# Optimization experiments

Hardware: AMD Instinct MI355X
Metric: run time of the kernel (lower is better)

The kernel has to match this reference:

```python
import jax, jax.numpy as jnp
import numpy as np

D_MODEL = 512
NHEAD = 8
HEAD_DIM = D_MODEL // NHEAD
D_FF = 2048
EPS = 1e-5


def _layernorm(x, w, b):
    mu = jnp.mean(x, axis=-1, keepdims=True)
    var = jnp.mean(jnp.square(x - mu), axis=-1, keepdims=True)
    return (x - mu) * jax.lax.rsqrt(var + EPS) * w + b


def setup_inputs() -> dict:
    key = jax.random.key(0)
    ks = jax.random.split(key, 10)
    B, L = 4, 2048
    x = jax.random.normal(ks[0], (B, L, D_MODEL), dtype=jnp.float32)
    attn_bias = jax.random.normal(ks[1], (1, NHEAD, L, L), dtype=jnp.float32)
    s = 0.02
    # weights stored as (in, out): y = x @ w + b
    wq = jax.random.normal(ks[2], (D_MODEL, D_MODEL), dtype=jnp.float32) * s
    wk = jax.random.normal(ks[3], (D_MODEL, D_MODEL), dtype=jnp.float32) * s
    wv = jax.random.normal(ks[4], (D_MODEL, D_MODEL), dtype=jnp.float32) * s
    wo = jax.random.normal(ks[5], (D_MODEL, D_MODEL), dtype=jnp.float32) * s
    w1 = jax.random.normal(ks[6], (D_MODEL, D_FF), dtype=jnp.float32) * s
    w2 = jax.random.normal(ks[7], (D_FF, D_MODEL), dtype=jnp.float32) * s
    z = lambda n: jnp.zeros((n,), dtype=jnp.float32)
    o = lambda n: jnp.ones((n,), dtype=jnp.float32)
    return {
        "x": x, "attn_bias": attn_bias,
        "ln1_w": o(D_MODEL), "ln1_b": z(D_MODEL),
        "ln2_w": o(D_MODEL), "ln2_b": z(D_MODEL),
        "wq": wq, "bq": z(D_MODEL), "wk": wk, "bk": z(D_MODEL),
        "wv": wv, "bv": z(D_MODEL), "wo": wo, "bo": z(D_MODEL),
        "w1": w1, "b1": z(D_FF), "w2": w2, "b2": z(D_MODEL),
    }


def reference(x, attn_bias, ln1_w, ln1_b, ln2_w, ln2_b,
              wq, bq, wk, bk, wv, bv, wo, bo, w1, b1, w2, b2):
    B, L, D = x.shape
    H, Dh = NHEAD, HEAD_DIM

    # --- self-attention block (pre-LN) ---
    h = _layernorm(x, ln1_w, ln1_b)
    q = (h @ wq + bq).reshape(B, L, H, Dh)
    k = (h @ wk + bk).reshape(B, L, H, Dh)
    v = (h @ wv + bv).reshape(B, L, H, Dh)
    scores = jnp.einsum('bqhd,bkhd->bhqk', q, k) * (Dh ** -0.5)
    scores = scores + attn_bias  # broadcast over batch if bias has leading 1
    attn = jax.nn.softmax(scores, axis=-1)
    o = jnp.einsum('bhqk,bkhd->bqhd', attn, v).reshape(B, L, D)
    x = x + (o @ wo + bo)

    # --- feed-forward block (pre-LN, exact GELU like torch nn.GELU) ---
    h2 = _layernorm(x, ln2_w, ln2_b)
    ff = jax.nn.gelu(h2 @ w1 + b1, approximate=False) @ w2 + b2
    return x + ff
```

## Files before the change

kernel.cpp:

```cpp
#include <hip/hip_runtime.h>
#include <hip/hip_bf16.h>

typedef __bf16 bf16x8 __attribute__((ext_vector_type(8)));
typedef float  f32x4  __attribute__((ext_vector_type(4)));
typedef unsigned short us8 __attribute__((ext_vector_type(8)));

__device__ inline unsigned short f2bf(float f) {
    unsigned u = __builtin_bit_cast(unsigned, f);
    u += 0x7fffu + ((u >> 16) & 1u);
    return (unsigned short)(u >> 16);
}

__device__ inline bf16x8 load_frag(const unsigned short* p) {
    return *reinterpret_cast<const bf16x8*>(p);
}

__device__ inline void gload_lds16(const unsigned short* g, unsigned short* l) {
    __builtin_amdgcn_global_load_lds(
        (const __attribute__((address_space(1))) void*)g,
        (__attribute__((address_space(3))) void*)l, 16, 0, 0);
}

__global__ void prep_kernel(const float* __restrict__ wq, const float* __restrict__ wk,
                            const float* __restrict__ wv, const float* __restrict__ wo,
                            const float* __restrict__ w1, const float* __restrict__ w2,
                            const float* __restrict__ bq, const float* __restrict__ bk,
                            const float* __restrict__ bv,
                            unsigned short* __restrict__ wqkvT, unsigned short* __restrict__ woT,
                            unsigned short* __restrict__ w1T, unsigned short* __restrict__ w2T,
                            float* __restrict__ biasqkv) {
    int bid = blockIdx.x;
    int tx = threadIdx.x, ty = threadIdx.y;
    if (bid >= 3072) {
        int i = (bid - 3072) * 256 + ty * 32 + tx;
        float v = (i < 512) ? bq[i] : ((i < 1024) ? bk[i - 512] : bv[i - 1024]);
        biasqkv[i] = v;
        return;
    }
    const float* src; unsigned short* dst; int K, N, tile;
    if (bid < 256)       { src = wq; dst = wqkvT;          K = 512;  N = 512;  tile = bid; }
    else if (bid < 512)  { src = wk; dst = wqkvT + 262144; K = 512;  N = 512;  tile = bid - 256; }
    else if (bid < 768)  { src = wv; dst = wqkvT + 524288; K = 512;  N = 512;  tile = bid - 512; }
    else if (bid < 1024) { src = wo; dst = woT;            K = 512;  N = 512;  tile = bid - 768; }
    else if (bid < 2048) { src = w1; dst = w1T;            K = 512;  N = 2048; tile = bid - 1024; }
    else                 { src = w2; dst = w2T;            K = 2048; N = 512;  tile = bid - 2048; }
    int ntx = N >> 5;
    int n0 = (tile % ntx) * 32, k0 = (tile / ntx) * 32;
    __shared__ float tilebuf[32][33];
#pragma unroll
    for (int i = 0; i < 4; ++i)
        tilebuf[ty + 8 * i][tx] = src[(size_t)(k0 + ty + 8 * i) * N + n0 + tx];
    __syncthreads();
#pragma unroll
    for (int i = 0; i < 4; ++i)
        dst[(size_t)(n0 + ty + 8 * i) * K + k0 + tx] = f2bf(tilebuf[tx][ty + 8 * i]);
}

__global__ __launch_bounds__(256) void ln_kernel(const float* __restrict__ x,
                                                 const float* __restrict__ w,
                                                 const float* __restrict__ b,
                                                 unsigned short* __restrict__ out) {
    int wave = threadIdx.x >> 6, lane = threadIdx.x & 63;
    size_t row = (size_t)blockIdx.x * 4 + wave;
    const float* xp = x + row * 512 + lane * 8;
    float4 v0 = *reinterpret_cast<const float4*>(xp);
    float4 v1 = *reinterpret_cast<const float4*>(xp + 4);
    float s = (v0.x + v0.y) + (v0.z + v0.w) + (v1.x + v1.y) + (v1.z + v1.w);
    float qq = v0.x * v0.x + v0.y * v0.y + v0.z * v0.z + v0.w * v0.w
             + v1.x * v1.x + v1.y * v1.y + v1.z * v1.z + v1.w * v1.w;
#pragma unroll
    for (int off = 1; off < 64; off <<= 1) {
        s += __shfl_xor(s, off, 64);
        qq += __shfl_xor(qq, off, 64);
    }
    float mu = s * (1.0f / 512.0f);
    float var = qq * (1.0f / 512.0f) - mu * mu;
    float rstd = rsqrtf(var + 1e-5f);
    int c = lane * 8;
    float4 w0 = *reinterpret_cast<const float4*>(w + c);
    float4 w1 = *reinterpret_cast<const float4*>(w + c + 4);
    float4 b0 = *reinterpret_cast<const float4*>(b + c);
    float4 b1 = *reinterpret_cast<const float4*>(b + c + 4);
    us8 r;
    r[0] = f2bf((v0.x - mu) * rstd * w0.x + b0.x);
    r[1] = f2bf((v0.y - mu) * rstd * w0.y + b0.y);
    r[2] = f2bf((v0.z - mu) * rstd * w0.z + b0.z);
    r[3] = f2bf((v0.w - mu) * rstd * w0.w + b0.w);
    r[4] = f2bf((v1.x - mu) * rstd * w1.x + b1.x);
    r[5] = f2bf((v1.y - mu) * rstd * w1.y + b1.y);
    r[6] = f2bf((v1.z - mu) * rstd * w1.z + b1.z);
    r[7] = f2bf((v1.w - mu) * rstd * w1.w + b1.w);
    *reinterpret_cast<us8*>(out + row * 512 + c) = r;
}

__device__ __forceinline__ void gemm_core(const unsigned short* __restrict__ A,
                                          const unsigned short* __restrict__ BT,
                                          int K, int ksteps,
                                          int m0, int n0, f32x4 (&acc)[4][4]) {
    __shared__ unsigned short As[8192];
    __shared__ unsigned short Bs[8192];
    const int tid = threadIdx.x;
    const int lane = tid & 63, wave = tid >> 6;
    const int quad = lane >> 4, l16 = lane & 15;
    const int wm = (wave >> 1) * 64, wn = (wave & 1) * 64;
    const int row0 = tid >> 3;
    const int jl = (tid & 7) ^ (row0 & 7);
    const unsigned short* ag = A + (size_t)(m0 + row0) * K + jl * 8;
    const unsigned short* bg = BT + (size_t)(n0 + row0) * K + jl * 8;
    unsigned short* al = As + tid * 8;
    unsigned short* bl = Bs + tid * 8;
    const int sw = l16 & 7;

    for (int ks = 0; ks < ksteps; ++ks) {
        __syncthreads();
#pragma unroll
        for (int s = 0; s < 4; ++s) {
            gload_lds16(ag + (size_t)32 * s * K, al + 2048 * s);
            gload_lds16(bg + (size_t)32 * s * K, bl + 2048 * s);
        }
        ag += 64; bg += 64;
        __syncthreads();
#pragma unroll
        for (int h = 0; h < 2; ++h) {
            bf16x8 af[4], bf[4];
#pragma unroll
            for (int i = 0; i < 4; ++i)
                af[i] = load_frag(As + (wm + i * 16 + l16) * 64 + (((h * 4 + quad) ^ sw) * 8));
#pragma unroll
            for (int j = 0; j < 4; ++j)
                bf[j] = load_frag(Bs + (wn + j * 16 + l16) * 64 + (((h * 4 + quad) ^ sw) * 8));
#pragma unroll
            for (int i = 0; i < 4; ++i)
#pragma unroll
                for (int j = 0; j < 4; ++j)
                    acc[i][j] = __builtin_amdgcn_mfma_f32_16x16x32_bf16(af[i], bf[j], acc[i][j], 0, 0, 0);
        }
    }
}

__device__ __forceinline__ void gemm_core_n64(const unsigned short* __restrict__ A,
                                              const unsigned short* __restrict__ BT,
                                              int K, int ksteps,
                                              int m0, int n0, f32x4 (&acc)[2][4]) {
    __shared__ unsigned short As[8192];
    __shared__ unsigned short Bs[4096];
    const int tid = threadIdx.x;
    const int lane = tid & 63, wave = tid >> 6;
    const int quad = lane >> 4, l16 = lane & 15;
    const int wm = wave * 32;
    const int row0 = tid >> 3;
    const int jl = (tid & 7) ^ (row0 & 7);
    const unsigned short* ag = A + (size_t)(m0 + row0) * K + jl * 8;
    const unsigned short* bg = BT + (size_t)(n0 + (row0 & 31)) * K + jl * 8;
    unsigned short* al = As + tid * 8;
    unsigned short* bl = Bs + tid * 8;
    const bool bstage = (row0 < 32);
    (void)bstage;
    const int sw = l16 & 7;

    for (int ks = 0; ks < ksteps; ++ks) {
        __syncthreads();
#pragma unroll
        for (int s = 0; s < 4; ++s)
            gload_lds16(ag + (size_t)32 * s * K, al + 2048 * s);
#pragma unroll
        for (int s = 0; s < 2; ++s)
            gload_lds16(bg + (size_t)32 * s * K, bl + 2048 * s);
        ag += 64; bg += 64;
        __syncthreads();
#pragma unroll
        for (int h = 0; h < 2; ++h) {
            bf16x8 af[2], bf[4];
#pragma unroll
            for (int i = 0; i < 2; ++i)
                af[i] = load_frag(As + (wm + i * 16 + l16) * 64 + (((h * 4 + quad) ^ sw) * 8));
#pragma unroll
            for (int j = 0; j < 4; ++j)
                bf[j] = load_frag(Bs + (j * 16 + l16) * 64 + (((h * 4 + quad) ^ sw) * 8));
#pragma unroll
            for (int i = 0; i < 2; ++i)
#pragma unroll
                for (int j = 0; j < 4; ++j)
                    acc[i][j] = __builtin_amdgcn_mfma_f32_16x16x32_bf16(af[i], bf[j], acc[i][j], 0, 0, 0);
        }
    }
}


__global__ __launch_bounds__(256) void gemm_oproj(const unsigned short* __restrict__ A,
                                                  const unsigned short* __restrict__ BT,
                                                  const float* __restrict__ bias,
                                                  const float* __restrict__ res,
                                                  float* __restrict__ C) {
    f32x4 acc[2][4] = {};
    const int m0 = blockIdx.y * 128, n0 = blockIdx.x * 64;
    gemm_core_n64(A, BT, 512, 8, m0, n0, acc);
    const int tid = threadIdx.x, lane = tid & 63, wave = tid >> 6;
    const int quad = lane >> 4, l16 = lane & 15;
    const int wm = wave * 32;
#pragma unroll
    for (int i = 0; i < 2; ++i)
#pragma unroll
        for (int j = 0; j < 4; ++j) {
            int n = n0 + j * 16 + l16;
            float bn = bias[n];
#pragma unroll
            for (int r = 0; r < 4; ++r) {
                int m = m0 + wm + i * 16 + quad * 4 + r;
                size_t idx = (size_t)m * 512 + n;
                C[idx] = acc[i][j][r] + bn + res[idx];
            }
        }
}

__global__ __launch_bounds__(256) void gemm_ff2(const unsigned short* __restrict__ A,
                                                const unsigned short* __restrict__ BT,
                                                const float* __restrict__ bias,
                                                float* __restrict__ C) {
    f32x4 acc[2][4] = {};
    const int m0 = blockIdx.y * 128, n0 = blockIdx.x * 64;
    gemm_core_n64(A, BT, 2048, 32, m0, n0, acc);
    const int tid = threadIdx.x, lane = tid & 63, wave = tid >> 6;
    const int quad = lane >> 4, l16 = lane & 15;
    const int wm = wave * 32;
#pragma unroll
    for (int i = 0; i < 2; ++i)
#pragma unroll
        for (int j = 0; j < 4; ++j) {
            int n = n0 + j * 16 + l16;
            float bn = bias[n];
#pragma unroll
            for (int r = 0; r < 4; ++r) {
                int m = m0 + wm + i * 16 + quad * 4 + r;
                size_t idx = (size_t)m * 512 + n;
                C[idx] = C[idx] + acc[i][j][r] + bn;
            }
        }
}

__global__ __launch_bounds__(256) void gemm_qkv_k(const unsigned short* __restrict__ A,
                                                  const unsigned short* __restrict__ BT,
                                                  const float* __restrict__ bias,
                                                  unsigned short* __restrict__ qk,
                                                  unsigned short* __restrict__ vT) {
    f32x4 acc[4][4] = {};
    const int m0 = blockIdx.y * 128, n0 = blockIdx.x * 128;
    gemm_core(A, BT, 512, 8, m0, n0, acc);
    const int tid = threadIdx.x, lane = tid & 63, wave = tid >> 6;
    const int quad = lane >> 4, l16 = lane & 15;
    const int wm = (wave >> 1) * 64, wn = (wave & 1) * 64;
    if (n0 < 1024) {
#pragma unroll
        for (int i = 0; i < 4; ++i)
#pragma unroll
            for (int j = 0; j < 4; ++j) {
                int n = n0 + wn + j * 16 + l16;
                float bn = bias[n];
#pragma unroll
                for (int r = 0; r < 4; ++r) {
                    int m = m0 + wm + i * 16 + quad * 4 + r;
                    qk[(size_t)m * 1024 + n] = f2bf(acc[i][j][r] + bn);
                }
            }
    } else {
#pragma unroll
        for (int i = 0; i < 4; ++i) {
            int mb = m0 + wm + i * 16 + quad * 4;
            int bb = mb >> 11, tok = mb & 2047;
#pragma unroll
            for (int j = 0; j < 4; ++j) {
                int n = n0 + wn + j * 16 + l16;
                float bn = bias[n];
                int hd = n - 1024;
                ushort4 pk;
                pk.x = f2bf(acc[i][j][0] + bn);
                pk.y = f2bf(acc[i][j][1] + bn);
                pk.z = f2bf(acc[i][j][2] + bn);
                pk.w = f2bf(acc[i][j][3] + bn);
                *reinterpret_cast<ushort4*>(vT + (size_t)(bb * 512 + hd) * 2048 + tok) = pk;
            }
        }
    }
}

__global__ __launch_bounds__(256) void gemm_gelu_k(const unsigned short* __restrict__ A,
                                                   const unsigned short* __restrict__ BT,
                                                   const float* __restrict__ bias,
                                                   unsigned short* __restrict__ C) {
    f32x4 acc[4][4] = {};
    const int m0 = blockIdx.y * 128, n0 = blockIdx.x * 128;
    gemm_core(A, BT, 512, 8, m0, n0, acc);
    const int tid = threadIdx.x, lane = tid & 63, wave = tid >> 6;
    const int quad = lane >> 4, l16 = lane & 15;
    const int wm = (wave >> 1) * 64, wn = (wave & 1) * 64;
#pragma unroll
    for (int i = 0; i < 4; ++i)
#pragma unroll
        for (int j = 0; j < 4; ++j) {
            int n = n0 + wn + j * 16 + l16;
            float bn = bias[n];
#pragma unroll
            for (int r = 0; r < 4; ++r) {
                int m = m0 + wm + i * 16 + quad * 4 + r;
                float val = acc[i][j][r] + bn;
                float g = 0.5f * val * (1.0f + erff(val * 0.70710678118654752f));
                C[(size_t)m * 2048 + n] = f2bf(g);
            }
        }
}

__global__ __launch_bounds__(256) void attn_kernel(const unsigned short* __restrict__ qk,
                                                   const unsigned short* __restrict__ vT,
                                                   const float* __restrict__ bias,
                                                   unsigned short* __restrict__ o) {
    __shared__ unsigned short Ks[2][2][4096];
    __shared__ unsigned short VTs[2][2][4096];
    __shared__ unsigned short Ps[2][4096];
    const int tid = threadIdx.x;
    const int lane = tid & 63, wave = tid >> 6, quad = lane >> 4, l16 = lane & 15;
    const int qb = blockIdx.x, h = blockIdx.y, bp = blockIdx.z;
    const int qw = qb * 64 + wave * 16;

    bf16x8 qf[2][2];
#pragma unroll
    for (int bi = 0; bi < 2; ++bi) {
        const unsigned short* qbase =
            qk + (size_t)((bp * 2 + bi) * 2048 + qw + l16) * 1024 + h * 64 + quad * 8;
        qf[bi][0] = load_frag(qbase);
        qf[bi][1] = load_frag(qbase + 32);
    }

    f32x4 Oacc[2][4] = {};
    float lsum[2][4] = {};

    const int p8 = lane & 7;
    const int r0 = wave * 16 + (lane >> 3);
    const int swz = (p8 ^ (r0 & 7)) * 8;
    const unsigned short* kg[2];
    const unsigned short* vg[2];
#pragma unroll
    for (int bi = 0; bi < 2; ++bi) {
        int b = bp * 2 + bi;
        kg[bi] = qk + (size_t)(b * 2048 + r0) * 1024 + 512 + h * 64 + swz;
        vg[bi] = vT + (size_t)(b * 512 + h * 64 + r0) * 2048 + swz;
    }
    const int ldst = r0 * 64 + p8 * 8;

    const float* brow = bias + (size_t)h * 2048 * 2048 + (size_t)(qw + quad * 4) * 2048 + l16;
    const float S2 = 0.18033688011112042f;
    const float K2 = 1.4426950408889634f;
    const float C2 = -11.541560327111707f;

#pragma unroll
    for (int bi = 0; bi < 2; ++bi) {
        gload_lds16(kg[bi], &Ks[0][bi][0] + ldst);
        gload_lds16(kg[bi] + 8 * 1024, &Ks[0][bi][512] + ldst);
        gload_lds16(vg[bi], &VTs[0][bi][0] + ldst);
        gload_lds16(vg[bi] + 8 * 2048, &VTs[0][bi][512] + ldst);
    }
    float bbf[4][4];
#pragma unroll
    for (int t = 0; t < 4; ++t)
#pragma unroll
        for (int r = 0; r < 4; ++r)
            bbf[t][r] = fmaf(brow[(size_t)r * 2048 + t * 16], K2, C2);

    const int sw7 = l16 & 7;
    for (int kt = 0; kt < 32; ++kt) {
        const int buf = kt & 1;
        __syncthreads();
        if (kt < 31) {
#pragma unroll
            for (int bi = 0; bi < 2; ++bi) {
                const unsigned short* kg2 = kg[bi] + (size_t)(kt + 1) * 64 * 1024;
                const unsigned short* vg2 = vg[bi] + (kt + 1) * 64;
                gload_lds16(kg2, &Ks[buf ^ 1][bi][0] + ldst);
                gload_lds16(kg2 + 8 * 1024, &Ks[buf ^ 1][bi][512] + ldst);
                gload_lds16(vg2, &VTs[buf ^ 1][bi][0] + ldst);
                gload_lds16(vg2 + 8 * 2048, &VTs[buf ^ 1][bi][512] + ldst);
            }
        }
#pragma unroll
        for (int bi = 0; bi < 2; ++bi) {
#pragma unroll
            for (int t = 0; t < 4; ++t) {
                const unsigned short* krow = &Ks[buf][bi][(t * 16 + l16) * 64];
                bf16x8 kb0 = load_frag(krow + ((quad ^ sw7) * 8));
                bf16x8 kb1 = load_frag(krow + (((quad + 4) ^ sw7) * 8));
                f32x4 c = {};
                c = __builtin_amdgcn_mfma_f32_16x16x32_bf16(qf[bi][0], kb0, c, 0, 0, 0);
                c = __builtin_amdgcn_mfma_f32_16x16x32_bf16(qf[bi][1], kb1, c, 0, 0, 0);
#pragma unroll
                for (int r = 0; r < 4; ++r) {
                    float e = __builtin_amdgcn_exp2f(fmaf(c[r], S2, bbf[t][r]));
                    lsum[bi][r] += e;
                    int m = quad * 4 + r;
                    int phys = (t * 2 + (l16 >> 3)) ^ ((m >> 1) & 7);
                    Ps[bi][wave * 1024 + m * 64 + phys * 8 + (l16 & 7)] = f2bf(e);
                }
            }
        }
        __syncthreads();
        if (kt < 31) {
            const float* b2 = brow + (size_t)(kt + 1) * 64;
#pragma unroll
            for (int t = 0; t < 4; ++t)
#pragma unroll
                for (int r = 0; r < 4; ++r)
                    bbf[t][r] = fmaf(b2[(size_t)r * 2048 + t * 16], K2, C2);
        }
#pragma unroll
        for (int bi = 0; bi < 2; ++bi) {
            const unsigned short* prow = &Ps[bi][wave * 1024 + l16 * 64];
            bf16x8 pa0 = load_frag(prow + ((quad ^ ((l16 >> 1) & 7)) * 8));
            bf16x8 pa1 = load_frag(prow + (((quad + 4) ^ ((l16 >> 1) & 7)) * 8));
#pragma unroll
            for (int t = 0; t < 4; ++t) {
                const unsigned short* vrow = &VTs[buf][bi][(t * 16 + l16) * 64];
                bf16x8 vb0 = load_frag(vrow + ((quad ^ sw7) * 8));
                bf16x8 vb1 = load_frag(vrow + (((quad + 4) ^ sw7) * 8));
                Oacc[bi][t] = __builtin_amdgcn_mfma_f32_16x16x32_bf16(pa0, vb0, Oacc[bi][t], 0, 0, 0);
                Oacc[bi][t] = __builtin_amdgcn_mfma_f32_16x16x32_bf16(pa1, vb1, Oacc[bi][t], 0, 0, 0);
            }
        }
    }

#pragma unroll
    for (int off = 1; off < 16; off <<= 1)
#pragma unroll
        for (int bi = 0; bi < 2; ++bi)
#pragma unroll
            for (int r = 0; r < 4; ++r) lsum[bi][r] += __shfl_xor(lsum[bi][r], off, 64);
#pragma unroll
    for (int bi = 0; bi < 2; ++bi)
#pragma unroll
        for (int r = 0; r < 4; ++r) {
            float inv = 1.0f / lsum[bi][r];
            int qg = qw + quad * 4 + r;
            unsigned short* op = o + (size_t)((bp * 2 + bi) * 2048 + qg) * 512 + h * 64;
#pragma unroll
            for (int t = 0; t < 4; ++t) op[t * 16 + l16] = f2bf(Oacc[bi][t][r] * inv);
        }
}

extern "C" void kernel_launch(void* const* d_in, const int* in_sizes, int n_in,
                              void* d_out, int out_size, void* d_ws, size_t ws_size,
                              hipStream_t stream) {
    const float* x      = (const float*)d_in[0];
    const float* abias  = (const float*)d_in[1];
    const float* ln1_w  = (const float*)d_in[2];
    const float* ln1_b  = (const float*)d_in[3];
    const float* ln2_w  = (const float*)d_in[4];
    const float* ln2_b  = (const float*)d_in[5];
    const float* wq     = (const float*)d_in[6];
    const float* bq     = (const float*)d_in[7];
    const float* wk     = (const float*)d_in[8];
    const float* bk     = (const float*)d_in[9];
    const float* wv     = (const float*)d_in[10];
    const float* bv     = (const float*)d_in[11];
    const float* wo     = (const float*)d_in[12];
    const float* bo     = (const float*)d_in[13];
    const float* w1     = (const float*)d_in[14];
    const float* b1     = (const float*)d_in[15];
    const float* w2     = (const float*)d_in[16];
    const float* b2     = (const float*)d_in[17];
    float* out = (float*)d_out;

    char* ws = (char*)d_ws;
    unsigned short* wqkvT  = (unsigned short*)(ws + 0);
    unsigned short* woT    = (unsigned short*)(ws + 1572864);
    unsigned short* w1T    = (unsigned short*)(ws + 2097152);
    unsigned short* w2T    = (unsigned short*)(ws + 4194304);
    float*          biasqkv= (float*)(ws + 6291456);
    unsigned short* hbuf   = (unsigned short*)(ws + 6297600);
    unsigned short* qkbuf  = (unsigned short*)(ws + 14686208);
    unsigned short* vTbuf  = (unsigned short*)(ws + 31463424);
    unsigned short* o_attn = (unsigned short*)(ws + 39852032);
    unsigned short* ff1    = (unsigned short*)(ws + 48240640);

    prep_kernel<<<3078, dim3(32, 8), 0, stream>>>(wq, wk, wv, wo, w1, w2, bq, bk, bv,
                                                  wqkvT, woT, w1T, w2T, biasqkv);
    ln_kernel<<<2048, 256, 0, stream>>>(x, ln1_w, ln1_b, hbuf);
    gemm_qkv_k<<<dim3(12, 64), 256, 0, stream>>>(hbuf, wqkvT, biasqkv, qkbuf, vTbuf);
    attn_kernel<<<dim3(32, 8, 2), 256, 0, stream>>>(qkbuf, vTbuf, abias, o_attn);
    gemm_oproj<<<dim3(8, 64), 256, 0, stream>>>(o_attn, woT, bo, x, out);
    ln_kernel<<<2048, 256, 0, stream>>>(out, ln2_w, ln2_b, hbuf);
    gemm_gelu_k<<<dim3(16, 64), 256, 0, stream>>>(hbuf, w1T, b1, ff1);
    gemm_ff2<<<dim3(8, 64), 256, 0, stream>>>(ff1, w2T, b2, out);
}
```

Before: 417.0 us.

## Double-buffer GEMM LDS tiles with prefetch and relax an attention barrier

Both GEMM cores switch from a single 64-wide K tile staged between two barriers per step to two 32-wide K buffers. The next tile is prefetched with direct global-to-LDS loads while MFMAs run on the current one, leaving one barrier per step. The LDS layout and XOR swizzle change to fit 32-element rows, and all callers double their step counts. In attention, one __syncthreads becomes a barrier that waits only on LDS counters, so outstanding global loads are not drained there. The price is twice as many loop iterations with half the MFMA work in each, and correctness now depends on the later full barrier catching the in-flight loads.

New measurement: 449.6 us. 1.08x slower.

```diff
diff --git a/kernel.cpp b/kernel.cpp
--- a/kernel.cpp
+++ b/kernel.cpp
@@ -19,6 +19,10 @@
     __builtin_amdgcn_global_load_lds(
         (const __attribute__((address_space(1))) void*)g,
         (__attribute__((address_space(3))) void*)l, 16, 0, 0);
+}
+
+__device__ inline void barrier_lds_only() {
+    asm volatile("s_waitcnt lgkmcnt(0)\ns_barrier" ::: "memory");
 }
 
 __global__ void prep_kernel(const float* __restrict__ wq, const float* __restrict__ wk,
@@ -97,44 +101,47 @@
                                           const unsigned short* __restrict__ BT,
                                           int K, int ksteps,
                                           int m0, int n0, f32x4 (&acc)[4][4]) {
-    __shared__ unsigned short As[8192];
-    __shared__ unsigned short Bs[8192];
+    __shared__ unsigned short As[2][4096];
+    __shared__ unsigned short Bs[2][4096];
     const int tid = threadIdx.x;
     const int lane = tid & 63, wave = tid >> 6;
     const int quad = lane >> 4, l16 = lane & 15;
     const int wm = (wave >> 1) * 64, wn = (wave & 1) * 64;
-    const int row0 = tid >> 3;
-    const int jl = (tid & 7) ^ (row0 & 7);
-    const unsigned short* ag = A + (size_t)(m0 + row0) * K + jl * 8;
-    const unsigned short* bg = BT + (size_t)(n0 + row0) * K + jl * 8;
-    unsigned short* al = As + tid * 8;
-    unsigned short* bl = Bs + tid * 8;
-    const int sw = l16 & 7;
+    const int c0 = tid, c1 = tid + 256;
+    const unsigned short* ag0 = A + (size_t)(m0 + (c0 >> 2)) * K + ((c0 & 3) ^ ((c0 >> 2) & 3)) * 8;
+    const unsigned short* ag1 = A + (size_t)(m0 + (c1 >> 2)) * K + ((c1 & 3) ^ ((c1 >> 2) & 3)) * 8;
+    const unsigned short* bg0 = BT + (size_t)(n0 + (c0 >> 2)) * K + ((c0 & 3) ^ ((c0 >> 2) & 3)) * 8;
+    const unsigned short* bg1 = BT + (size_t)(n0 + (c1 >> 2)) * K + ((c1 & 3) ^ ((c1 >> 2) & 3)) * 8;
+    const int l0 = c0 * 8, l1 = c1 * 8;
+    const int sw = (quad ^ (l16 & 3)) * 8;
+
+    gload_lds16(ag0, &As[0][0] + l0);
+    gload_lds16(ag1, &As[0][0] + l1);
+    gload_lds16(bg0, &Bs[0][0] + l0);
+    gload_lds16(bg1, &Bs[0][0] + l1);
 
     for (int ks = 0; ks < ksteps; ++ks) {
+        const int buf = ks & 1;
         __syncthreads();
-#pragma unroll
-        for (int s = 0; s < 4; ++s) {
-            gload_lds16(ag + (size_t)32 * s * K, al + 2048 * s);
-            gload_lds16(bg + (size_t)32 * s * K, bl + 2048 * s);
-        }
-        ag += 64; bg += 64;
-        __syncthreads();
-#pragma unroll
-        for (int h = 0; h < 2; ++h) {
-            bf16x8 af[4], bf[4];
-#pragma unroll
-            for (int i = 0; i < 4; ++i)
-                af[i] = load_frag(As + (wm + i * 16 + l16) * 64 + (((h * 4 + quad) ^ sw) * 8));
+        if (ks + 1 < ksteps) {
+            const int ko = (ks + 1) * 32;
+            gload_lds16(ag0 + ko, &As[buf ^ 1][0] + l0);
+            gload_lds16(ag1 + ko, &As[buf ^ 1][0] + l1);
+            gload_lds16(bg0 + ko, &Bs[buf ^ 1][0] + l0);
+            gload_lds16(bg1 + ko, &Bs[buf ^ 1][0] + l1);
+        }
+        bf16x8 af[4], bf[4];
+#pragma unroll
+        for (int i = 0; i < 4; ++i)
+            af[i] = load_frag(&As[buf][(wm + i * 16 + l16) * 32] + sw);
+#pragma unroll
+        for (int j = 0; j < 4; ++j)
+            bf[j] = load_frag(&Bs[buf][(wn + j * 16 + l16) * 32] + sw);
+#pragma unroll
+        for (int i = 0; i < 4; ++i)
 #pragma unroll
             for (int j = 0; j < 4; ++j)
-                bf[j] = load_frag(Bs + (wn + j * 16 + l16) * 64 + (((h * 4 + quad) ^ sw) * 8));
-#pragma unroll
-            for (int i = 0; i < 4; ++i)
-#pragma unroll
-                for (int j = 0; j < 4; ++j)
-                    acc[i][j] = __builtin_amdgcn_mfma_f32_16x16x32_bf16(af[i], bf[j], acc[i][j], 0, 0, 0);
-        }
+                acc[i][j] = __builtin_amdgcn_mfma_f32_16x16x32_bf16(af[i], bf[j], acc[i][j], 0, 0, 0);
     }
 }
 
@@ -142,50 +149,46 @@
                                               const unsigned short* __restrict__ BT,
                                               int K, int ksteps,
                                               int m0, int n0, f32x4 (&acc)[2][4]) {
-    __shared__ unsigned short As[8192];
-    __shared__ unsigned short Bs[4096];
+    __shared__ unsigned short As[2][4096];
+    __shared__ unsigned short Bs[2][2048];
     const int tid = threadIdx.x;
     const int lane = tid & 63, wave = tid >> 6;
     const int quad = lane >> 4, l16 = lane & 15;
     const int wm = wave * 32;
-    const int row0 = tid >> 3;
-    const int jl = (tid & 7) ^ (row0 & 7);
-    const unsigned short* ag = A + (size_t)(m0 + row0) * K + jl * 8;
-    const unsigned short* bg = BT + (size_t)(n0 + (row0 & 31)) * K + jl * 8;
-    unsigned short* al = As + tid * 8;
-    unsigned short* bl = Bs + tid * 8;
-    const bool bstage = (row0 < 32);
-    (void)bstage;
-    const int sw = l16 & 7;
+    const int c0 = tid, c1 = tid + 256;
+    const unsigned short* ag0 = A + (size_t)(m0 + (c0 >> 2)) * K + ((c0 & 3) ^ ((c0 >> 2) & 3)) * 8;
+    const unsigned short* ag1 = A + (size_t)(m0 + (c1 >> 2)) * K + ((c1 & 3) ^ ((c1 >> 2) & 3)) * 8;
+    const unsigned short* bg0 = BT + (size_t)(n0 + (c0 >> 2)) * K + ((c0 & 3) ^ ((c0 >> 2) & 3)) * 8;
+    const int l0 = c0 * 8, l1 = c1 * 8;
+    const int sw = (quad ^ (l16 & 3)) * 8;
+
+    gload_lds16(ag0, &As[0][0] + l0);
+    gload_lds16(ag1, &As[0][0] + l1);
+    gload_lds16(bg0, &Bs[0][0] + l0);
 
     for (int ks = 0; ks < ksteps; ++ks) {
+        const int buf = ks & 1;
         __syncthreads();
-#pragma unroll
-        for (int s = 0; s < 4; ++s)
-            gload_lds16(ag + (size_t)32 * s * K, al + 2048 * s);
-#pragma unroll
-        for (int s = 0; s < 2; ++s)
-            gload_lds16(bg + (size_t)32 * s * K, bl + 2048 * s);
-        ag += 64; bg += 64;
-        __syncthreads();
-#pragma unroll
-        for (int h = 0; h < 2; ++h) {
-            bf16x8 af[2], bf[4];
-#pragma unroll
-            for (int i = 0; i < 2; ++i)
-                af[i] = load_frag(As + (wm + i * 16 + l16) * 64 + (((h * 4 + quad) ^ sw) * 8));
+        if (ks + 1 < ksteps) {
+            const int ko = (ks + 1) * 32;
+            gload_lds16(ag0 + ko, &As[buf ^ 1][0] + l0);
+            gload_lds16(ag1 + ko, &As[buf ^ 1][0] + l1);
+            gload_lds16(bg0 + ko, &Bs[buf ^ 1][0] + l0);
+        }
+        bf16x8 af[2], bf[4];
+#pragma unroll
+        for (int i = 0; i < 2; ++i)
+            af[i] = load_frag(&As[buf][(wm + i * 16 + l16) * 32] + sw);
+#pragma unroll
+        for (int j = 0; j < 4; ++j)
+            bf[j] = load_frag(&Bs[buf][(j * 16 + l16) * 32] + sw);
+#pragma unroll
+        for (int i = 0; i < 2; ++i)
 #pragma unroll
             for (int j = 0; j < 4; ++j)
-                bf[j] = load_frag(Bs + (j * 16 + l16) * 64 + (((h * 4 + quad) ^ sw) * 8));
-#pragma unroll
-            for (int i = 0; i < 2; ++i)
-#pragma unroll
-                for (int j = 0; j < 4; ++j)
-                    acc[i][j] = __builtin_amdgcn_mfma_f32_16x16x32_bf16(af[i], bf[j], acc[i][j], 0, 0, 0);
-        }
-    }
-}
-
+                acc[i][j] = __builtin_amdgcn_mfma_f32_16x16x32_bf16(af[i], bf[j], acc[i][j], 0, 0, 0);
+    }
+}
 
 __global__ __launch_bounds__(256) void gemm_oproj(const unsigned short* __restrict__ A,
                                                   const unsigned short* __restrict__ BT,
@@ -194,7 +197,7 @@
                                                   float* __restrict__ C) {
     f32x4 acc[2][4] = {};
     const int m0 = blockIdx.y * 128, n0 = blockIdx.x * 64;
-    gemm_core_n64(A, BT, 512, 8, m0, n0, acc);
+    gemm_core_n64(A, BT, 512, 16, m0, n0, acc);
     const int tid = threadIdx.x, lane = tid & 63, wave = tid >> 6;
     const int quad = lane >> 4, l16 = lane & 15;
     const int wm = wave * 32;
@@ -219,7 +222,7 @@
                                                 float* __restrict__ C) {
     f32x4 acc[2][4] = {};
     const int m0 = blockIdx.y * 128, n0 = blockIdx.x * 64;
-    gemm_core_n64(A, BT, 2048, 32, m0, n0, acc);
+    gemm_core_n64(A, BT, 2048, 64, m0, n0, acc);
     const int tid = threadIdx.x, lane = tid & 63, wave = tid >> 6;
     const int quad = lane >> 4, l16 = lane & 15;
     const int wm = wave * 32;
@@ -245,7 +248,7 @@
                                                   unsigned short* __restrict__ vT) {
     f32x4 acc[4][4] = {};
     const int m0 = blockIdx.y * 128, n0 = blockIdx.x * 128;
-    gemm_core(A, BT, 512, 8, m0, n0, acc);
+    gemm_core(A, BT, 512, 16, m0, n0, acc);
     const int tid = threadIdx.x, lane = tid & 63, wave = tid >> 6;
     const int quad = lane >> 4, l16 = lane & 15;
     const int wm = (wave >> 1) * 64, wn = (wave & 1) * 64;
@@ -289,7 +292,7 @@
                                                    unsigned short* __restrict__ C) {
     f32x4 acc[4][4] = {};
     const int m0 = blockIdx.y * 128, n0 = blockIdx.x * 128;
-    gemm_core(A, BT, 512, 8, m0, n0, acc);
+    gemm_core(A, BT, 512, 16, m0, n0, acc);
     const int tid = threadIdx.x, lane = tid & 63, wave = tid >> 6;
     const int quad = lane >> 4, l16 = lane & 15;
     const int wm = (wave >> 1) * 64, wn = (wave & 1) * 64;
@@ -400,7 +403,7 @@
                 }
             }
         }
-        __syncthreads();
+        barrier_lds_only();
         if (kt < 31) {
             const float* b2 = brow + (size_t)(kt + 1) * 64;
 #pragma unroll
```

## Split attention blocks per batch, relax barrier, enlarge GELU GEMM tile

Applied to the files above, without the earlier changes.

The attention kernel now handles one batch per block instead of two, doubling the grid and halving the LDS per block. Batch is the fastest grid dimension so blocks sharing an attention-bias tile run close together and can reuse it from cache. The barrier after writing P now waits only on LDS counters, so in-flight K/V prefetches are not drained early. The FF1+GELU GEMM moves to 512-thread blocks with 256x128 tiles to reuse each B tile across more rows, at the cost of more LDS and registers per block and more bias traffic from DRAM if cache reuse fails.

Measured after the change: 451.1 us. 8.2% more time.

```diff
diff --git a/kernel.cpp b/kernel.cpp
--- a/kernel.cpp
+++ b/kernel.cpp
@@ -19,6 +19,10 @@
     __builtin_amdgcn_global_load_lds(
         (const __attribute__((address_space(1))) void*)g,
         (__attribute__((address_space(3))) void*)l, 16, 0, 0);
+}
+
+__device__ inline void barrier_lds_only() {
+    asm volatile("s_waitcnt lgkmcnt(0)\ns_barrier" ::: "memory");
 }
 
 __global__ void prep_kernel(const float* __restrict__ wq, const float* __restrict__ wk,
@@ -138,6 +142,52 @@
     }
 }
 
+__device__ __forceinline__ void gemm_core_256(const unsigned short* __restrict__ A,
+                                              const unsigned short* __restrict__ BT,
+                                              int K, int ksteps,
+                                              int m0, int n0, f32x4 (&acc)[4][4]) {
+    __shared__ unsigned short As[16384];
+    __shared__ unsigned short Bs[8192];
+    const int tid = threadIdx.x;
+    const int lane = tid & 63, wave = tid >> 6;
+    const int quad = lane >> 4, l16 = lane & 15;
+    const int wm = (wave >> 1) * 64, wn = (wave & 1) * 64;
+    const int row0 = tid >> 3;
+    const int jl = (tid & 7) ^ (row0 & 7);
+    const unsigned short* ag = A + (size_t)(m0 + row0) * K + jl * 8;
+    const unsigned short* bg = BT + (size_t)(n0 + row0) * K + jl * 8;
+    unsigned short* al = As + tid * 8;
+    unsigned short* bl = Bs + tid * 8;
+    const int sw = l16 & 7;
+
+    for (int ks = 0; ks < ksteps; ++ks) {
+        __syncthreads();
+#pragma unroll
+        for (int s = 0; s < 4; ++s)
+            gload_lds16(ag + (size_t)64 * s * K, al + 4096 * s);
+#pragma unroll
+        for (int s = 0; s < 2; ++s)
+            gload_lds16(bg + (size_t)64 * s * K, bl + 4096 * s);
+        ag += 64; bg += 64;
+        __syncthreads();
+#pragma unroll
+        for (int h = 0; h < 2; ++h) {
+            bf16x8 af[4], bf[4];
+#pragma unroll
+            for (int i = 0; i < 4; ++i)
+                af[i] = load_frag(As + (wm + i * 16 + l16) * 64 + (((h * 4 + quad) ^ sw) * 8));
+#pragma unroll
+            for (int j = 0; j < 4; ++j)
+                bf[j] = load_frag(Bs + (wn + j * 16 + l16) * 64 + (((h * 4 + quad) ^ sw) * 8));
+#pragma unroll
+            for (int i = 0; i < 4; ++i)
+#pragma unroll
+                for (int j = 0; j < 4; ++j)
+                    acc[i][j] = __builtin_amdgcn_mfma_f32_16x16x32_bf16(af[i], bf[j], acc[i][j], 0, 0, 0);
+        }
+    }
+}
+
 __device__ __forceinline__ void gemm_core_n64(const unsigned short* __restrict__ A,
                                               const unsigned short* __restrict__ BT,
                                               int K, int ksteps,
@@ -154,8 +204,6 @@
     const unsigned short* bg = BT + (size_t)(n0 + (row0 & 31)) * K + jl * 8;
     unsigned short* al = As + tid * 8;
     unsigned short* bl = Bs + tid * 8;
-    const bool bstage = (row0 < 32);
-    (void)bstage;
     const int sw = l16 & 7;
 
     for (int ks = 0; ks < ksteps; ++ks) {
@@ -185,7 +233,6 @@
         }
     }
 }
-
 
 __global__ __launch_bounds__(256) void gemm_oproj(const unsigned short* __restrict__ A,
                                                   const unsigned short* __restrict__ BT,
@@ -283,13 +330,13 @@
     }
 }
 
-__global__ __launch_bounds__(256) void gemm_gelu_k(const unsigned short* __restrict__ A,
+__global__ __launch_bounds__(512) void gemm_gelu_k(const unsigned short* __restrict__ A,
                                                    const unsigned short* __restrict__ BT,
                                                    const float* __restrict__ bias,
                                                    unsigned short* __restrict__ C) {
     f32x4 acc[4][4] = {};
-    const int m0 = blockIdx.y * 128, n0 = blockIdx.x * 128;
-    gemm_core(A, BT, 512, 8, m0, n0, acc);
+    const int m0 = blockIdx.y * 256, n0 = blockIdx.x * 128;
+    gemm_core_256(A, BT, 512, 8, m0, n0, acc);
     const int tid = threadIdx.x, lane = tid & 63, wave = tid >> 6;
     const int quad = lane >> 4, l16 = lane & 15;
     const int wm = (wave >> 1) * 64, wn = (wave & 1) * 64;
@@ -313,37 +360,26 @@
                                                    const unsigned short* __restrict__ vT,
                                                    const float* __restrict__ bias,
                                                    unsigned short* __restrict__ o) {
-    __shared__ unsigned short Ks[2][2][4096];
-    __shared__ unsigned short VTs[2][2][4096];
-    __shared__ unsigned short Ps[2][4096];
+    __shared__ unsigned short Ks[2][4096];
+    __shared__ unsigned short VTs[2][4096];
+    __shared__ unsigned short Ps[4096];
     const int tid = threadIdx.x;
     const int lane = tid & 63, wave = tid >> 6, quad = lane >> 4, l16 = lane & 15;
-    const int qb = blockIdx.x, h = blockIdx.y, bp = blockIdx.z;
+    const int b = blockIdx.x, qb = blockIdx.y, h = blockIdx.z;
     const int qw = qb * 64 + wave * 16;
 
-    bf16x8 qf[2][2];
-#pragma unroll
-    for (int bi = 0; bi < 2; ++bi) {
-        const unsigned short* qbase =
-            qk + (size_t)((bp * 2 + bi) * 2048 + qw + l16) * 1024 + h * 64 + quad * 8;
-        qf[bi][0] = load_frag(qbase);
-        qf[bi][1] = load_frag(qbase + 32);
-    }
-
-    f32x4 Oacc[2][4] = {};
-    float lsum[2][4] = {};
+    const unsigned short* qbase = qk + (size_t)(b * 2048 + qw + l16) * 1024 + h * 64 + quad * 8;
+    bf16x8 qf0 = load_frag(qbase);
+    bf16x8 qf1 = load_frag(qbase + 32);
+
+    f32x4 Oacc[4] = {};
+    float lsum[4] = {};
 
     const int p8 = lane & 7;
     const int r0 = wave * 16 + (lane >> 3);
     const int swz = (p8 ^ (r0 & 7)) * 8;
-    const unsigned short* kg[2];
-    const unsigned short* vg[2];
-#pragma unroll
-    for (int bi = 0; bi < 2; ++bi) {
-        int b = bp * 2 + bi;
-        kg[bi] = qk + (size_t)(b * 2048 + r0) * 1024 + 512 + h * 64 + swz;
-        vg[bi] = vT + (size_t)(b * 512 + h * 64 + r0) * 2048 + swz;
-    }
+    const unsigned short* kg = qk + (size_t)(b * 2048 + r0) * 1024 + 512 + h * 64 + swz;
+    const unsigned short* vg = vT + (size_t)(b * 512 + h * 64 + r0) * 2048 + swz;
     const int ldst = r0 * 64 + p8 * 8;
 
     const float* brow = bias + (size_t)h * 2048 * 2048 + (size_t)(qw + quad * 4) * 2048 + l16;
@@ -351,13 +387,10 @@
     const float K2 = 1.4426950408889634f;
     const float C2 = -11.541560327111707f;
 
-#pragma unroll
-    for (int bi = 0; bi < 2; ++bi) {
-        gload_lds16(kg[bi], &Ks[0][bi][0] + ldst);
-        gload_lds16(kg[bi] + 8 * 1024, &Ks[0][bi][512] + ldst);
-        gload_lds16(vg[bi], &VTs[0][bi][0] + ldst);
-        gload_lds16(vg[bi] + 8 * 2048, &VTs[0][bi][512] + ldst);
-    }
+    gload_lds16(kg, Ks[0] + ldst);
+    gload_lds16(kg + 8 * 1024, Ks[0] + 512 + ldst);
+    gload_lds16(vg, VTs[0] + ldst);
+    gload_lds16(vg + 8 * 2048, VTs[0] + 512 + ldst);
     float bbf[4][4];
 #pragma unroll
     for (int t = 0; t < 4; ++t)
@@ -370,37 +403,31 @@
         const int buf = kt & 1;
         __syncthreads();
         if (kt < 31) {
-#pragma unroll
-            for (int bi = 0; bi < 2; ++bi) {
-                const unsigned short* kg2 = kg[bi] + (size_t)(kt + 1) * 64 * 1024;
-                const unsigned short* vg2 = vg[bi] + (kt + 1) * 64;
-                gload_lds16(kg2, &Ks[buf ^ 1][bi][0] + ldst);
-                gload_lds16(kg2 + 8 * 1024, &Ks[buf ^ 1][bi][512] + ldst);
-                gload_lds16(vg2, &VTs[buf ^ 1][bi][0] + ldst);
-                gload_lds16(vg2 + 8 * 2048, &VTs[buf ^ 1][bi][512] + ldst);
+            const unsigned short* kg2 = kg + (size_t)(kt + 1) * 64 * 1024;
+            const unsigned short* vg2 = vg + (kt + 1) * 64;
+            gload_lds16(kg2, Ks[buf ^ 1] + ldst);
+            gload_lds16(kg2 + 8 * 1024, Ks[buf ^ 1] + 512 + ldst);
+            gload_lds16(vg2, VTs[buf ^ 1] + ldst);
+            gload_lds16(vg2 + 8 * 2048, VTs[buf ^ 1] + 512 + ldst);
+        }
+#pragma unroll
+        for (int t = 0; t < 4; ++t) {
+            const unsigned short* krow = Ks[buf] + (t * 16 + l16) * 64;
+            bf16x8 kb0 = load_frag(krow + ((quad ^ sw7) * 8));
+            bf16x8 kb1 = load_frag(krow + (((quad + 4) ^ sw7) * 8));
+            f32x4 c = {};
+            c = __builtin_amdgcn_mfma_f32_16x16x32_bf16(qf0, kb0, c, 0, 0, 0);
+            c = __builtin_amdgcn_mfma_f32_16x16x32_bf16(qf1, kb1, c, 0, 0, 0);
+#pragma unroll
+            for (int r = 0; r < 4; ++r) {
+                float e = __builtin_amdgcn_exp2f(fmaf(c[r], S2, bbf[t][r]));
+                lsum[r] += e;
+                int m = quad * 4 + r;
+                int phys = (t * 2 + (l16 >> 3)) ^ ((m >> 1) & 7);
+                Ps[wave * 1024 + m * 64 + phys * 8 + (l16 & 7)] = f2bf(e);
             }
         }
-#pragma unroll
-        for (int bi = 0; bi < 2; ++bi) {
-#pragma unroll
-            for (int t = 0; t < 4; ++t) {
-                const unsigned short* krow = &Ks[buf][bi][(t * 16 + l16) * 64];
-                bf16x8 kb0 = load_frag(krow + ((quad ^ sw7) * 8));
-                bf16x8 kb1 = load_frag(krow + (((quad + 4) ^ sw7) * 8));
-                f32x4 c = {};
-                c = __builtin_amdgcn_mfma_f32_16x16x32_bf16(qf[bi][0], kb0, c, 0, 0, 0);
-                c = __builtin_amdgcn_mfma_f32_16x16x32_bf16(qf[bi][1], kb1, c, 0, 0, 0);
-#pragma unroll
-                for (int r = 0; r < 4; ++r) {
-                    float e = __builtin_amdgcn_exp2f(fmaf(c[r], S2, bbf[t][r]));
-                    lsum[bi][r] += e;
-                    int m = quad * 4 + r;
-                    int phys = (t * 2 + (l16 >> 3)) ^ ((m >> 1) & 7);
-                    Ps[bi][wave * 1024 + m * 64 + phys * 8 + (l16 & 7)] = f2bf(e);
-                }
-            }
-        }
-        __syncthreads();
+        barrier_lds_only();
         if (kt < 31) {
             const float* b2 = brow + (size_t)(kt + 1) * 64;
 #pragma unroll
@@ -409,38 +436,31 @@
                 for (int r = 0; r < 4; ++r)
                     bbf[t][r] = fmaf(b2[(size_t)r * 2048 + t * 16], K2, C2);
         }
-#pragma unroll
-        for (int bi = 0; bi < 2; ++bi) {
-            const unsigned short* prow = &Ps[bi][wave * 1024 + l16 * 64];
-            bf16x8 pa0 = load_frag(prow + ((quad ^ ((l16 >> 1) & 7)) * 8));
-            bf16x8 pa1 = load_frag(prow + (((quad + 4) ^ ((l16 >> 1) & 7)) * 8));
-#pragma unroll
-            for (int t = 0; t < 4; ++t) {
-                const unsigned short* vrow = &VTs[buf][bi][(t * 16 + l16) * 64];
-                bf16x8 vb0 = load_frag(vrow + ((quad ^ sw7) * 8));
-                bf16x8 vb1 = load_frag(vrow + (((quad + 4) ^ sw7) * 8));
-                Oacc[bi][t] = __builtin_amdgcn_mfma_f32_16x16x32_bf16(pa0, vb0, Oacc[bi][t], 0, 0, 0);
-                Oacc[bi][t] = __builtin_amdgcn_mfma_f32_16x16x32_bf16(pa1, vb1, Oacc[bi][t], 0, 0, 0);
-            }
+        const unsigned short* prow = Ps + wave * 1024 + l16 * 64;
+        bf16x8 pa0 = load_frag(prow + ((quad ^ ((l16 >> 1) & 7)) * 8));
+        bf16x8 pa1 = load_frag(prow + (((quad + 4) ^ ((l16 >> 1) & 7)) * 8));
+#pragma unroll
+        for (int t = 0; t < 4; ++t) {
+            const unsigned short* vrow = VTs[buf] + (t * 16 + l16) * 64;
+            bf16x8 vb0 = load_frag(vrow + ((quad ^ sw7) * 8));
+            bf16x8 vb1 = load_frag(vrow + (((quad + 4) ^ sw7) * 8));
+            Oacc[t] = __builtin_amdgcn_mfma_f32_16x16x32_bf16(pa0, vb0, Oacc[t], 0, 0, 0);
+            Oacc[t] = __builtin_amdgcn_mfma_f32_16x16x32_bf16(pa1, vb1, Oacc[t], 0, 0, 0);
         }
     }
 
 #pragma unroll
     for (int off = 1; off < 16; off <<= 1)
 #pragma unroll
-        for (int bi = 0; bi < 2; ++bi)
-#pragma unroll
-            for (int r = 0; r < 4; ++r) lsum[bi][r] += __shfl_xor(lsum[bi][r], off, 64);
-#pragma unroll
-    for (int bi = 0; bi < 2; ++bi)
-#pragma unroll
-        for (int r = 0; r < 4; ++r) {
-            float inv = 1.0f / lsum[bi][r];
-            int qg = qw + quad * 4 + r;
-            unsigned short* op = o + (size_t)((bp * 2 + bi) * 2048 + qg) * 512 + h * 64;
-#pragma unroll
-            for (int t = 0; t < 4; ++t) op[t * 16 + l16] = f2bf(Oacc[bi][t][r] * inv);
-        }
+        for (int r = 0; r < 4; ++r) lsum[r] += __shfl_xor(lsum[r], off, 64);
+#pragma unroll
+    for (int r = 0; r < 4; ++r) {
+        float inv = 1.0f / lsum[r];
+        int qg = qw + quad * 4 + r;
+        unsigned short* op = o + (size_t)(b * 2048 + qg) * 512 + h * 64;
+#pragma unroll
+        for (int t = 0; t < 4; ++t) op[t * 16 + l16] = f2bf(Oacc[t][r] * inv);
+    }
 }
 
 extern "C" void kernel_launch(void* const* d_in, const int* in_sizes, int n_in,
@@ -482,9 +502,9 @@
                                                   wqkvT, woT, w1T, w2T, biasqkv);
     ln_kernel<<<2048, 256, 0, stream>>>(x, ln1_w, ln1_b, hbuf);
     gemm_qkv_k<<<dim3(12, 64), 256, 0, stream>>>(hbuf, wqkvT, biasqkv, qkbuf, vTbuf);
-    attn_kernel<<<dim3(32, 8, 2), 256, 0, stream>>>(qkbuf, vTbuf, abias, o_attn);
+    attn_kernel<<<dim3(4, 32, 8), 256, 0, stream>>>(qkbuf, vTbuf, abias, o_attn);
     gemm_oproj<<<dim3(8, 64), 256, 0, stream>>>(o_attn, woT, bo, x, out);
     ln_kernel<<<2048, 256, 0, stream>>>(out, ln2_w, ln2_b, hbuf);
-    gemm_gelu_k<<<dim3(16, 64), 256, 0, stream>>>(hbuf, w1T, b1, ff1);
+    gemm_gelu_k<<<dim3(16, 32), 512, 0, stream>>>(hbuf, w1T, b1, ff1);
     gemm_ff2<<<dim3(8, 64), 256, 0, stream>>>(ff1, w2T, b2, out);
 }
```
